# Kernel tuning notes

Measured on AMD Instinct MI355X. Metric: run time of the kernel, lower is better.

The kernel has to match this reference:

```python
import jax, jax.numpy as jnp
import numpy as np

N, B, NG = 12288, 8, 1536   # total nodes, graphs, nodes per graph
E, T, R, H = 49152, 9, 4, 128  # edges, node types, edge types, hidden

def setup_inputs() -> dict:
    key = jax.random.key(0)
    ks = jax.random.split(key, 24)
    s = 0.05
    inp = {
        'n_feats': jax.random.uniform(ks[0], (N, T), jnp.float32),
        'eps': jax.random.normal(ks[1], (N, H), jnp.float32),
        'edge_src': jax.random.randint(ks[2], (E,), 0, N, jnp.int32),
        'edge_dst': jax.random.randint(ks[3], (E,), 0, N, jnp.int32),
        'e_types': jax.random.randint(ks[4], (E,), 0, R, jnp.int32),
        # RelGraphConv params: per-relation weight, self-loop weight, bias
        'W1': jax.random.normal(ks[5], (R, T, H)) * s,  'Ws1': jax.random.normal(ks[6], (T, H)) * s,  'b1': jnp.zeros((H,)),
        'W2': jax.random.normal(ks[7], (R, H, H)) * s,  'Ws2': jax.random.normal(ks[8], (H, H)) * s,  'b2': jnp.zeros((H,)),
        'Wmu': jax.random.normal(ks[9], (R, H, H)) * s, 'Wsmu': jax.random.normal(ks[10], (H, H)) * s, 'bmu': jnp.zeros((H,)),
        'Wls': jax.random.normal(ks[11], (R, H, H)) * s, 'Wsls': jax.random.normal(ks[12], (H, H)) * s, 'bls': jnp.zeros((H,)),
        # decoder heads
        'Wnt': jax.random.normal(ks[13], (H, T)) * s, 'bnt': jnp.zeros((T,)),
        'we': jax.random.normal(ks[14], (3 * H + 2 * T,)) * s, 'be': jnp.zeros(()),
        'Wt': jax.random.normal(ks[15], (3 * H + 2 * T, R)) * s, 'bt': jnp.zeros((R,)),
    }
    return inp

def _relconv(h, W, Wself, b, edge_src, edge_dst, e_types):
    # per-relation transform then gather per edge: avoids [E,d,d] weight gather
    hr = jnp.einsum('nd,rdk->rnk', h, W)          # [R,N,H]
    msgs = hr[e_types, edge_src]                   # [E,H]
    agg = jax.ops.segment_sum(msgs, edge_dst, num_segments=N)
    return agg + h @ Wself + b

def reference(n_feats, eps, edge_src, edge_dst, e_types,
              W1, Ws1, b1, W2, Ws2, b2, Wmu, Wsmu, bmu, Wls, Wsls, bls,
              Wnt, bnt, we, be, Wt, bt):
    # ---- encode ----
    h = jax.nn.relu(_relconv(n_feats, W1, Ws1, b1, edge_src, edge_dst, e_types))
    h = jax.nn.relu(_relconv(h, W2, Ws2, b2, edge_src, edge_dst, e_types))
    mu = _relconv(h, Wmu, Wsmu, bmu, edge_src, edge_dst, e_types)
    logstd = _relconv(h, Wls, Wsls, bls, edge_src, edge_dst, e_types)
    z = mu + eps * jnp.exp(logstd)                 # reparameterize
    gz = z.reshape(B, NG, H).mean(axis=1)          # per-graph mean readout [B,H]

    # ---- decode (batched pairwise MLP) ----
    nt = z @ Wnt + bnt                             # [N,T]
    # edge_existence_fc on concat(u_z,u_t,v_z,v_t,gz) decomposes rank-1:
    wu_z, wu_t = we[:H], we[H:H + T]
    wv_z, wv_t = we[H + T:2 * H + T], we[2 * H + T:2 * H + 2 * T]
    wg = we[2 * H + 2 * T:]
    su = (z @ wu_z + nt @ wu_t).reshape(B, NG)     # [B,n]
    sv = (z @ wv_z + nt @ wv_t).reshape(B, NG)
    sg = gz @ wg + be                              # [B]
    exist = jax.nn.sigmoid(su[:, :, None] + sv[:, None, :] + sg[:, None, None])  # [B,n,n]

    Au = (z @ Wt[:H] + nt @ Wt[H:H + T]).reshape(B, NG, R)
    Av = (z @ Wt[H + T:2 * H + T] + nt @ Wt[2 * H + T:2 * H + 2 * T]).reshape(B, NG, R)
    Ag = gz @ Wt[2 * H + 2 * T:] + bt              # [B,R]
    type_logits = Au[:, :, None, :] + Av[:, None, :, :] + Ag[:, None, None, :]  # [B,n,n,R]

    pair_out = jnp.concatenate([exist[..., None], type_logits], axis=-1)  # [B,n,n,1+R]
    return pair_out, nt, mu, logstd
```

## Files before the change

kernel.cpp:

```cpp
#include <hip/hip_runtime.h>

#define NN 12288
#define TT 9
#define RR 4
#define HH 128
#define EE 49152
#define BB 8
#define NGG 1536
#define CAP 16

typedef unsigned short u16;
typedef float float4_t __attribute__((ext_vector_type(4)));
typedef __bf16 bf16x8 __attribute__((ext_vector_type(8)));
typedef unsigned short ushort8_t __attribute__((ext_vector_type(8)));

__device__ __forceinline__ u16 f2bf(float f) {
    union { float f; unsigned int u; } x; x.f = f;
    unsigned int r = x.u + 0x7FFFu + ((x.u >> 16) & 1u);
    return (u16)(r >> 16);
}
__device__ __forceinline__ float bf2f(u16 h) {
    union { unsigned int u; float f; } x; x.u = ((unsigned int)h) << 16; return x.f;
}

__global__ __launch_bounds__(256) void build_wts(
    const float* __restrict__ W1, const float* __restrict__ Ws1,
    const float* __restrict__ W2, const float* __restrict__ Ws2,
    const float* __restrict__ Wmu, const float* __restrict__ Wsmu,
    const float* __restrict__ Wls, const float* __restrict__ Wsls,
    u16* __restrict__ Bt1, u16* __restrict__ Bt2, u16* __restrict__ Bt34,
    int* __restrict__ cnt, float* __restrict__ gzacc)
{
    const int L1 = 128 * 64;
    const int L2 = L1 + 128 * 640;
    const int L3 = L2 + 256 * 640;
    const int L4 = L3 + NN * RR;
    const int L5 = L4 + BB * HH;
    int idx = blockIdx.x * 256 + threadIdx.x;
    if (idx < L1) {
        int k = idx >> 6, kk = idx & 63;
        float v = 0.f;
        if (kk < 36)      v = W1[kk * HH + k];
        else if (kk < 45) v = Ws1[(kk - 36) * HH + k];
        Bt1[k * 64 + kk] = f2bf(v);
    } else if (idx < L2) {
        int i2 = idx - L1;
        int k = i2 / 640, kk = i2 - k * 640;
        float v = (kk < 512) ? W2[kk * HH + k] : Ws2[(kk - 512) * HH + k];
        Bt2[k * 640 + kk] = f2bf(v);
    } else if (idx < L3) {
        int i3 = idx - L2;
        int j = i3 / 640, kk = i3 - j * 640;
        float v;
        if (j < 128) v = (kk < 512) ? Wmu[kk * HH + j] : Wsmu[(kk - 512) * HH + j];
        else { int jj = j - 128; v = (kk < 512) ? Wls[kk * HH + jj] : Wsls[(kk - 512) * HH + jj]; }
        Bt34[j * 640 + kk] = f2bf(v);
    } else if (idx < L4) {
        cnt[idx - L3] = 0;
    } else if (idx < L5) {
        gzacc[idx - L4] = 0.f;
    }
}

__global__ __launch_bounds__(256) void bucket_build(
    const int* __restrict__ esrc, const int* __restrict__ edst,
    const int* __restrict__ etyp, int* __restrict__ cnt, u16* __restrict__ buck)
{
    int e = blockIdx.x * 256 + threadIdx.x;
    if (e >= EE) return;
    int b = edst[e] * RR + etyp[e];
    int idx = atomicAdd(&cnt[b], 1);
    if (idx < CAP) buck[b * CAP + idx] = (u16)esrc[e];
}

__global__ __launch_bounds__(256) void gatherA1(
    const int* __restrict__ cnt, const u16* __restrict__ buck,
    const float* __restrict__ feats, u16* __restrict__ A)
{
    int idx = blockIdx.x * 256 + threadIdx.x;
    int n = idx >> 6, c = idx & 63;
    float v = 0.f;
    if (c < 36) {
        int r = c / 9, t = c - r * 9;
        int b = n * RR + r;
        int m = cnt[b]; m = m > CAP ? CAP : m;
        const u16* bp = buck + b * CAP;
        for (int i = 0; i < m; ++i) v += feats[(int)bp[i] * TT + t];
    } else if (c < 45) {
        v = feats[n * TT + (c - 36)];
    }
    A[(size_t)n * 64 + c] = f2bf(v);
}

__global__ __launch_bounds__(256) void gatherA2(
    const int* __restrict__ cnt, const u16* __restrict__ buck,
    const u16* __restrict__ h, u16* __restrict__ A)
{
    int n = blockIdx.x;
    u16* Ar = A + (size_t)n * 640;
    __shared__ int scnt[RR];
    __shared__ u16 ssrc[RR * CAP];
    if (threadIdx.x < RR) {
        int m = cnt[n * RR + threadIdx.x];
        scnt[threadIdx.x] = m > CAP ? CAP : m;
    }
    if (threadIdx.x < RR * CAP) ssrc[threadIdx.x] = buck[n * RR * CAP + threadIdx.x];
    __syncthreads();
    for (int c = threadIdx.x; c < 640; c += 256) {
        u16 v;
        if (c < 512) {
            int r = c >> 7, k = c & 127;
            float acc = 0.f;
            int m = scnt[r];
            for (int i = 0; i < m; ++i)
                acc += bf2f(h[(size_t)ssrc[r * CAP + i] * HH + k]);
            v = f2bf(acc);
        } else {
            v = h[(size_t)n * HH + (c - 512)];
        }
        Ar[c] = v;
    }
}

template <int MODE>
__global__ __launch_bounds__(256) void gemm_k(
    const u16* __restrict__ A, const u16* __restrict__ Bt, int K,
    const float* __restrict__ bias_a, const float* __restrict__ bias_b,
    u16* __restrict__ outb, float* __restrict__ outf_a, float* __restrict__ outf_b)
{
    __shared__ __align__(16) u16 lds_a[64 * 40];
    __shared__ __align__(16) u16 lds_b[128 * 40];
    const int tid = threadIdx.x;
    const int w = tid >> 6, lane = tid & 63;
    const int m0 = blockIdx.x * 64;
    const int n0 = blockIdx.y * 128;
    const int wm = (w & 1) * 32, wn = (w >> 1) * 64;
    const int lm = lane & 15, lq = lane >> 4;

    float4_t acc[2][4];
#pragma unroll
    for (int i = 0; i < 2; ++i)
#pragma unroll
        for (int j = 0; j < 4; ++j) acc[i][j] = (float4_t){0.f, 0.f, 0.f, 0.f};

    const int arow = tid >> 2, akc = (tid & 3) * 8;
    const int nsteps = K >> 5;
    for (int kt = 0; kt < nsteps; ++kt) {
        int k0 = kt * 32;
        *(ushort8_t*)&lds_a[arow * 40 + akc] =
            *(const ushort8_t*)&A[(size_t)(m0 + arow) * K + k0 + akc];
        {
            int c0 = tid;       int bn0 = c0 >> 2, bk0 = (c0 & 3) * 8;
            *(ushort8_t*)&lds_b[bn0 * 40 + bk0] =
                *(const ushort8_t*)&Bt[(size_t)(n0 + bn0) * K + k0 + bk0];
            int c1 = tid + 256; int bn1 = c1 >> 2, bk1 = (c1 & 3) * 8;
            *(ushort8_t*)&lds_b[bn1 * 40 + bk1] =
                *(const ushort8_t*)&Bt[(size_t)(n0 + bn1) * K + k0 + bk1];
        }
        __syncthreads();
        bf16x8 a0 = *(const bf16x8*)&lds_a[(wm + 0 * 16 + lm) * 40 + lq * 8];
        bf16x8 a1 = *(const bf16x8*)&lds_a[(wm + 1 * 16 + lm) * 40 + lq * 8];
        bf16x8 b0 = *(const bf16x8*)&lds_b[(wn + 0 * 16 + lm) * 40 + lq * 8];
        bf16x8 b1 = *(const bf16x8*)&lds_b[(wn + 1 * 16 + lm) * 40 + lq * 8];
        bf16x8 b2 = *(const bf16x8*)&lds_b[(wn + 2 * 16 + lm) * 40 + lq * 8];
        bf16x8 b3 = *(const bf16x8*)&lds_b[(wn + 3 * 16 + lm) * 40 + lq * 8];
        acc[0][0] = __builtin_amdgcn_mfma_f32_16x16x32_bf16(a0, b0, acc[0][0], 0, 0, 0);
        acc[0][1] = __builtin_amdgcn_mfma_f32_16x16x32_bf16(a0, b1, acc[0][1], 0, 0, 0);
        acc[0][2] = __builtin_amdgcn_mfma_f32_16x16x32_bf16(a0, b2, acc[0][2], 0, 0, 0);
        acc[0][3] = __builtin_amdgcn_mfma_f32_16x16x32_bf16(a0, b3, acc[0][3], 0, 0, 0);
        acc[1][0] = __builtin_amdgcn_mfma_f32_16x16x32_bf16(a1, b0, acc[1][0], 0, 0, 0);
        acc[1][1] = __builtin_amdgcn_mfma_f32_16x16x32_bf16(a1, b1, acc[1][1], 0, 0, 0);
        acc[1][2] = __builtin_amdgcn_mfma_f32_16x16x32_bf16(a1, b2, acc[1][2], 0, 0, 0);
        acc[1][3] = __builtin_amdgcn_mfma_f32_16x16x32_bf16(a1, b3, acc[1][3], 0, 0, 0);
        __syncthreads();
    }

#pragma unroll
    for (int i = 0; i < 2; ++i)
#pragma unroll
        for (int j = 0; j < 4; ++j) {
            int gn = n0 + wn + j * 16 + lm;
#pragma unroll
            for (int reg = 0; reg < 4; ++reg) {
                int gm = m0 + wm + i * 16 + lq * 4 + reg;
                float v = acc[i][j][reg];
                if (MODE == 0) {
                    v += bias_a[gn];
                    v = v > 0.f ? v : 0.f;
                    outb[(size_t)gm * HH + gn] = f2bf(v);
                } else {
                    if (gn < HH) {
                        outf_a[(size_t)gm * HH + gn] = v + bias_a[gn];
                    } else {
                        int g2 = gn - HH;
                        outf_b[(size_t)gm * HH + g2] = v + bias_b[g2];
                    }
                }
            }
        }
}

__global__ __launch_bounds__(256) void node_epi(
    const float* __restrict__ mu, const float* __restrict__ ls,
    const float* __restrict__ eps,
    const float* __restrict__ Wnt, const float* __restrict__ bnt,
    const float* __restrict__ we, const float* __restrict__ Wt,
    float* __restrict__ out_nt,
    float* __restrict__ su, float* __restrict__ sv,
    float* __restrict__ Au, float* __restrict__ Av,
    float* __restrict__ gzacc)
{
    __shared__ float zs[64][129];
    __shared__ float nts[64][10];
    __shared__ float red[256];
    const int nb = blockIdx.x * 64;
    const int tid = threadIdx.x;

    for (int i = tid; i < 64 * 32; i += 256) {
        int n = i >> 5, c4 = (i & 31) * 4;
        size_t g = (size_t)(nb + n) * HH + c4;
        float4_t m4 = *(const float4_t*)&mu[g];
        float4_t l4 = *(const float4_t*)&ls[g];
        float4_t e4 = *(const float4_t*)&eps[g];
        float* zp = &zs[n][c4];
#pragma unroll
        for (int j = 0; j < 4; ++j) zp[j] = m4[j] + e4[j] * __expf(l4[j]);
    }
    __syncthreads();

    for (int o = tid; o < 64 * TT; o += 256) {
        int n = o / TT, t = o - n * TT;
        float acc = bnt[t];
#pragma unroll 8
        for (int k = 0; k < HH; ++k) acc += zs[n][k] * Wnt[k * TT + t];
        nts[n][t] = acc;
        out_nt[(size_t)(nb + n) * TT + t] = acc;
    }
    __syncthreads();

    for (int o = tid; o < 64 * 10; o += 256) {
        int n = o / 10, j = o - n * 10;
        int zoff, toff;
        const float* wv;
        if (j == 0)      { zoff = 0;   toff = 128; wv = we; }
        else if (j == 1) { zoff = 137; toff = 265; wv = we; }
        else if (j < 6)  { zoff = 0;   toff = 128; wv = Wt + (j - 2); }
        else             { zoff = 137; toff = 265; wv = Wt + (j - 6); }
        int stride = (j < 2) ? 1 : 4;
        float acc = 0.f;
#pragma unroll 8
        for (int k = 0; k < HH; ++k) acc += zs[n][k] * wv[(zoff + k) * stride];
#pragma unroll
        for (int t = 0; t < TT; ++t) acc += nts[n][t] * wv[(toff + t) * stride];
        int gn = nb + n;
        if (j == 0)      su[gn] = acc;
        else if (j == 1) sv[gn] = acc;
        else if (j < 6)  Au[(size_t)gn * 4 + (j - 2)] = acc;
        else             Av[(size_t)gn * 4 + (j - 6)] = acc;
    }

    {
        int k = tid & 127, half = tid >> 7;
        float s = 0.f;
#pragma unroll 8
        for (int r = 0; r < 32; ++r) s += zs[half * 32 + r][k];
        red[tid] = s;
        __syncthreads();
        if (tid < 128) {
            int b = blockIdx.x / 24;
            atomicAdd(&gzacc[b * HH + tid], red[tid] + red[tid + 128]);
        }
    }
}

__global__ __launch_bounds__(128) void gz_final_kernel(
    const float* __restrict__ gzacc, const float* __restrict__ we,
    const float* __restrict__ Wt, const float* __restrict__ be,
    const float* __restrict__ bt, float* __restrict__ sg, float* __restrict__ Ag)
{
    int b = blockIdx.x, k = threadIdx.x;
    float gz = gzacc[b * HH + k] * (1.f / NGG);
    float vals[5] = { we[274 + k], Wt[(274 + k) * 4 + 0], Wt[(274 + k) * 4 + 1],
                      Wt[(274 + k) * 4 + 2], Wt[(274 + k) * 4 + 3] };
    __shared__ float red[128];
    for (int j = 0; j < 5; ++j) {
        red[k] = gz * vals[j];
        __syncthreads();
        for (int off = 64; off >= 1; off >>= 1) {
            if (k < off) red[k] += red[k + off];
            __syncthreads();
        }
        if (k == 0) {
            if (j == 0) sg[b] = red[0] + be[0];
            else        Ag[b * 4 + (j - 1)] = red[0] + bt[j - 1];
        }
        __syncthreads();
    }
}

__global__ __launch_bounds__(256) void pair_kernel(
    const float* __restrict__ su, const float* __restrict__ sv,
    const float* __restrict__ Au, const float* __restrict__ Av,
    const float* __restrict__ sg, const float* __restrict__ Ag,
    float* __restrict__ out)
{
    int row = blockIdx.x;
    int b = row / NGG;
    float su_u = su[row] + sg[b];
    float t0 = Au[(size_t)row * 4 + 0] + Ag[b * 4 + 0];
    float t1 = Au[(size_t)row * 4 + 1] + Ag[b * 4 + 1];
    float t2 = Au[(size_t)row * 4 + 2] + Ag[b * 4 + 2];
    float t3 = Au[(size_t)row * 4 + 3] + Ag[b * 4 + 3];
    const float* svb = sv + (size_t)b * NGG;
    const float* avb = Av + (size_t)b * NGG * 4;
    float4_t* od = (float4_t*)(out + (size_t)row * 7680);
    for (int d = threadIdx.x; d < 1920; d += 256) {
        float4_t vv;
#pragma unroll
        for (int j = 0; j < 4; ++j) {
            unsigned int e = (unsigned int)d * 4u + j;
            unsigned int v0 = (e * 52429u) >> 18;
            unsigned int c  = e - v0 * 5u;
            float f;
            if (c == 0u) { float x = su_u + svb[v0]; f = 1.f / (1.f + __expf(-x)); }
            else { float tv = (c == 1u) ? t0 : (c == 2u) ? t1 : (c == 3u) ? t2 : t3;
                   f = tv + avb[v0 * 4u + (c - 1u)]; }
            vv[j] = f;
        }
        __builtin_nontemporal_store(vv, &od[d]);
    }
}

extern "C" void kernel_launch(void* const* d_in, const int* in_sizes, int n_in,
                              void* d_out, int out_size, void* d_ws, size_t ws_size,
                              hipStream_t stream)
{
    const float* feats = (const float*)d_in[0];
    const float* eps   = (const float*)d_in[1];
    const int* esrc  = (const int*)d_in[2];
    const int* edst  = (const int*)d_in[3];
    const int* etyp  = (const int*)d_in[4];
    const float* W1    = (const float*)d_in[5];
    const float* Ws1   = (const float*)d_in[6];
    const float* b1    = (const float*)d_in[7];
    const float* W2    = (const float*)d_in[8];
    const float* Ws2   = (const float*)d_in[9];
    const float* b2    = (const float*)d_in[10];
    const float* Wmu   = (const float*)d_in[11];
    const float* Wsmu  = (const float*)d_in[12];
    const float* bmu   = (const float*)d_in[13];
    const float* Wls   = (const float*)d_in[14];
    const float* Wsls  = (const float*)d_in[15];
    const float* bls   = (const float*)d_in[16];
    const float* Wnt   = (const float*)d_in[17];
    const float* bnt   = (const float*)d_in[18];
    const float* we    = (const float*)d_in[19];
    const float* be    = (const float*)d_in[20];
    const float* Wt    = (const float*)d_in[21];
    const float* bt    = (const float*)d_in[22];

    char* p = (char*)d_ws;
    auto alloc = [&](size_t bytes) -> char* {
        char* r = p; p += (bytes + 255) & ~(size_t)255; return r;
    };
    u16*   Abuf  = (u16*)  alloc((size_t)NN * 640 * 2);
    u16*   hbf   = (u16*)  alloc((size_t)NN * HH * 2);
    int*   cnt   = (int*)  alloc((size_t)NN * RR * 4);
    u16*   buck  = (u16*)  alloc((size_t)NN * RR * CAP * 2);
    float* gzacc = (float*)alloc((size_t)BB * HH * 4);
    u16*   Bt1   = (u16*)  alloc(128 * 64 * 2);
    u16*   Bt2   = (u16*)  alloc(128 * 640 * 2);
    u16*   Bt34  = (u16*)  alloc(256 * 640 * 2);
    float* suA   = (float*)alloc(NN * 4);
    float* svA   = (float*)alloc(NN * 4);
    float* AuA   = (float*)alloc(NN * 4 * 4);
    float* AvA   = (float*)alloc(NN * 4 * 4);
    float* sgA   = (float*)alloc(BB * 4);
    float* AgA   = (float*)alloc(BB * 4 * 4);

    float* out = (float*)d_out;
    const size_t PO = (size_t)BB * NGG * NGG * 5;
    float* out_nt = out + PO;
    float* out_mu = out_nt + (size_t)NN * TT;
    float* out_ls = out_mu + (size_t)NN * HH;

    build_wts<<<1188, 256, 0, stream>>>(W1, Ws1, W2, Ws2, Wmu, Wsmu, Wls, Wsls,
                                        Bt1, Bt2, Bt34, cnt, gzacc);

    bucket_build<<<EE / 256, 256, 0, stream>>>(esrc, edst, etyp, cnt, buck);

    gatherA1<<<NN * 64 / 256, 256, 0, stream>>>(cnt, buck, feats, Abuf);
    gemm_k<0><<<dim3(NN / 64, 1), 256, 0, stream>>>(Abuf, Bt1, 64, b1, nullptr,
                                                    hbf, nullptr, nullptr);

    gatherA2<<<NN, 256, 0, stream>>>(cnt, buck, hbf, Abuf);
    gemm_k<0><<<dim3(NN / 64, 1), 256, 0, stream>>>(Abuf, Bt2, 640, b2, nullptr,
                                                    hbf, nullptr, nullptr);

    gatherA2<<<NN, 256, 0, stream>>>(cnt, buck, hbf, Abuf);
    gemm_k<1><<<dim3(NN / 64, 2), 256, 0, stream>>>(Abuf, Bt34, 640, bmu, bls,
                                                    nullptr, out_mu, out_ls);

    node_epi<<<NN / 64, 256, 0, stream>>>(out_mu, out_ls, eps, Wnt, bnt, we, Wt,
                                          out_nt, suA, svA, AuA, AvA, gzacc);

    gz_final_kernel<<<BB, 128, 0, stream>>>(gzacc, we, Wt, be, bt, sgA, AgA);
    pair_kernel<<<NN, 256, 0, stream>>>(suA, svA, AuA, AvA, sgA, AgA, out);
}
```

Baseline: 602.9 us.

## Fuse neighbor gather-aggregation into GEMM A-tile loads for all conv layers

Removes the separate gatherA1/gatherA2 kernels and the materialized [N,640] A buffer. Each GEMM block now stages bucket counts and source indices for its 64 rows in LDS and builds A tiles on the fly by summing neighbor rows of h, loading 8 bf16 values per neighbor. This avoids writing and re-reading the large A buffer and cuts kernel launches. In exchange the gather now sits inside the GEMM main loop without overlap and is redone by both column blocks of the mu/logstd GEMM. Ping-pong h buffers are added so a layer never reads the buffer it writes.

```diff
diff --git a/kernel.cpp b/kernel.cpp
--- a/kernel.cpp
+++ b/kernel.cpp
@@ -73,63 +73,114 @@
     if (idx < CAP) buck[b * CAP + idx] = (u16)esrc[e];
 }
 
-__global__ __launch_bounds__(256) void gatherA1(
+
+__global__ __launch_bounds__(256) void gemm_l1(
     const int* __restrict__ cnt, const u16* __restrict__ buck,
-    const float* __restrict__ feats, u16* __restrict__ A)
-{
-    int idx = blockIdx.x * 256 + threadIdx.x;
-    int n = idx >> 6, c = idx & 63;
-    float v = 0.f;
-    if (c < 36) {
-        int r = c / 9, t = c - r * 9;
-        int b = n * RR + r;
-        int m = cnt[b]; m = m > CAP ? CAP : m;
-        const u16* bp = buck + b * CAP;
-        for (int i = 0; i < m; ++i) v += feats[(int)bp[i] * TT + t];
-    } else if (c < 45) {
-        v = feats[n * TT + (c - 36)];
-    }
-    A[(size_t)n * 64 + c] = f2bf(v);
-}
-
-__global__ __launch_bounds__(256) void gatherA2(
+    const float* __restrict__ feats, const u16* __restrict__ Bt,
+    const float* __restrict__ bias, u16* __restrict__ outb)
+{
+    __shared__ __align__(16) u16 lds_a[64 * 40];
+    __shared__ __align__(16) u16 lds_b[128 * 40];
+    __shared__ int scnt[64 * RR];
+    __shared__ __align__(16) u16 ssrc[64 * RR * CAP];
+    const int tid = threadIdx.x;
+    const int w = tid >> 6, lane = tid & 63;
+    const int m0 = blockIdx.x * 64;
+    const int wm = (w & 1) * 32, wn = (w >> 1) * 64;
+    const int lm = lane & 15, lq = lane >> 4;
+
+    {
+        int m = cnt[m0 * RR + tid];
+        scnt[tid] = m > CAP ? CAP : m;
+        const ushort8_t* bs = (const ushort8_t*)(buck + (size_t)m0 * RR * CAP);
+        ushort8_t* bd = (ushort8_t*)ssrc;
+        bd[tid] = bs[tid];
+        bd[tid + 256] = bs[tid + 256];
+    }
+
+    float4_t acc[2][4];
+#pragma unroll
+    for (int i = 0; i < 2; ++i)
+#pragma unroll
+        for (int j = 0; j < 4; ++j) acc[i][j] = (float4_t){0.f, 0.f, 0.f, 0.f};
+
+    const int arow = tid >> 2, akc = (tid & 3) * 8;
+    __syncthreads();
+
+    for (int kt = 0; kt < 2; ++kt) {
+        int k0 = kt * 32;
+        {
+            ushort8_t av;
+#pragma unroll
+            for (int j = 0; j < 8; ++j) {
+                int c = k0 + akc + j;
+                float v = 0.f;
+                if (c < 36) {
+                    int r = (c >= 27) ? 3 : (c >= 18) ? 2 : (c >= 9) ? 1 : 0;
+                    int t = c - r * 9;
+                    int bi = arow * RR + r;
+                    int m = scnt[bi];
+                    const u16* sp = &ssrc[bi * CAP];
+                    for (int i = 0; i < m; ++i) v += feats[(int)sp[i] * TT + t];
+                } else if (c < 45) {
+                    v = feats[(m0 + arow) * TT + (c - 36)];
+                }
+                av[j] = f2bf(v);
+            }
+            *(ushort8_t*)&lds_a[arow * 40 + akc] = av;
+        }
+        {
+            int c0 = tid;       int bn0 = c0 >> 2, bk0 = (c0 & 3) * 8;
+            *(ushort8_t*)&lds_b[bn0 * 40 + bk0] =
+                *(const ushort8_t*)&Bt[(size_t)bn0 * 64 + k0 + bk0];
+            int c1 = tid + 256; int bn1 = c1 >> 2, bk1 = (c1 & 3) * 8;
+            *(ushort8_t*)&lds_b[bn1 * 40 + bk1] =
+                *(const ushort8_t*)&Bt[(size_t)bn1 * 64 + k0 + bk1];
+        }
+        __syncthreads();
+        bf16x8 a0 = *(const bf16x8*)&lds_a[(wm + 0 * 16 + lm) * 40 + lq * 8];
+        bf16x8 a1 = *(const bf16x8*)&lds_a[(wm + 1 * 16 + lm) * 40 + lq * 8];
+        bf16x8 b0 = *(const bf16x8*)&lds_b[(wn + 0 * 16 + lm) * 40 + lq * 8];
+        bf16x8 b1 = *(const bf16x8*)&lds_b[(wn + 1 * 16 + lm) * 40 + lq * 8];
+        bf16x8 b2 = *(const bf16x8*)&lds_b[(wn + 2 * 16 + lm) * 40 + lq * 8];
+        bf16x8 b3 = *(const bf16x8*)&lds_b[(wn + 3 * 16 + lm) * 40 + lq * 8];
+        acc[0][0] = __builtin_amdgcn_mfma_f32_16x16x32_bf16(a0, b0, acc[0][0], 0, 0, 0);
+        acc[0][1] = __builtin_amdgcn_mfma_f32_16x16x32_bf16(a0, b1, acc[0][1], 0, 0, 0);
+        acc[0][2] = __builtin_amdgcn_mfma_f32_16x16x32_bf16(a0, b2, acc[0][2], 0, 0, 0);
+        acc[0][3] = __builtin_amdgcn_mfma_f32_16x16x32_bf16(a0, b3, acc[0][3], 0, 0, 0);
+        acc[1][0] = __builtin_amdgcn_mfma_f32_16x16x32_bf16(a1, b0, acc[1][0], 0, 0, 0);
+        acc[1][1] = __builtin_amdgcn_mfma_f32_16x16x32_bf16(a1, b1, acc[1][1], 0, 0, 0);
+        acc[1][2] = __builtin_amdgcn_mfma_f32_16x16x32_bf16(a1, b2, acc[1][2], 0, 0, 0);
+        acc[1][3] = __builtin_amdgcn_mfma_f32_16x16x32_bf16(a1, b3, acc[1][3], 0, 0, 0);
+        __syncthreads();
+    }
+
+#pragma unroll
+    for (int i = 0; i < 2; ++i)
+#pragma unroll
+        for (int j = 0; j < 4; ++j) {
+            int gn = wn + j * 16 + lm;
+#pragma unroll
+            for (int reg = 0; reg < 4; ++reg) {
+                int gm = m0 + wm + i * 16 + lq * 4 + reg;
+                float v = acc[i][j][reg] + bias[gn];
+                v = v > 0.f ? v : 0.f;
+                outb[(size_t)gm * HH + gn] = f2bf(v);
+            }
+        }
+}
+
+template <int MODE>
+__global__ __launch_bounds__(256) void gemm_l23(
     const int* __restrict__ cnt, const u16* __restrict__ buck,
-    const u16* __restrict__ h, u16* __restrict__ A)
-{
-    int n = blockIdx.x;
-    u16* Ar = A + (size_t)n * 640;
-    __shared__ int scnt[RR];
-    __shared__ u16 ssrc[RR * CAP];
-    if (threadIdx.x < RR) {
-        int m = cnt[n * RR + threadIdx.x];
-        scnt[threadIdx.x] = m > CAP ? CAP : m;
-    }
-    if (threadIdx.x < RR * CAP) ssrc[threadIdx.x] = buck[n * RR * CAP + threadIdx.x];
-    __syncthreads();
-    for (int c = threadIdx.x; c < 640; c += 256) {
-        u16 v;
-        if (c < 512) {
-            int r = c >> 7, k = c & 127;
-            float acc = 0.f;
-            int m = scnt[r];
-            for (int i = 0; i < m; ++i)
-                acc += bf2f(h[(size_t)ssrc[r * CAP + i] * HH + k]);
-            v = f2bf(acc);
-        } else {
-            v = h[(size_t)n * HH + (c - 512)];
-        }
-        Ar[c] = v;
-    }
-}
-
-template <int MODE>
-__global__ __launch_bounds__(256) void gemm_k(
-    const u16* __restrict__ A, const u16* __restrict__ Bt, int K,
+    const u16* __restrict__ h, const u16* __restrict__ Bt,
     const float* __restrict__ bias_a, const float* __restrict__ bias_b,
     u16* __restrict__ outb, float* __restrict__ outf_a, float* __restrict__ outf_b)
 {
     __shared__ __align__(16) u16 lds_a[64 * 40];
     __shared__ __align__(16) u16 lds_b[128 * 40];
+    __shared__ int scnt[64 * RR];
+    __shared__ __align__(16) u16 ssrc[64 * RR * CAP];
     const int tid = threadIdx.x;
     const int w = tid >> 6, lane = tid & 63;
     const int m0 = blockIdx.x * 64;
@@ -137,6 +188,15 @@
     const int wm = (w & 1) * 32, wn = (w >> 1) * 64;
     const int lm = lane & 15, lq = lane >> 4;
 
+    {
+        int m = cnt[m0 * RR + tid];
+        scnt[tid] = m > CAP ? CAP : m;
+        const ushort8_t* bs = (const ushort8_t*)(buck + (size_t)m0 * RR * CAP);
+        ushort8_t* bd = (ushort8_t*)ssrc;
+        bd[tid] = bs[tid];
+        bd[tid + 256] = bs[tid + 256];
+    }
+
     float4_t acc[2][4];
 #pragma unroll
     for (int i = 0; i < 2; ++i)
@@ -144,11 +204,32 @@
         for (int j = 0; j < 4; ++j) acc[i][j] = (float4_t){0.f, 0.f, 0.f, 0.f};
 
     const int arow = tid >> 2, akc = (tid & 3) * 8;
-    const int nsteps = K >> 5;
-    for (int kt = 0; kt < nsteps; ++kt) {
+    const int K = 640;
+    __syncthreads();
+
+    for (int kt = 0; kt < 20; ++kt) {
         int k0 = kt * 32;
-        *(ushort8_t*)&lds_a[arow * 40 + akc] =
-            *(const ushort8_t*)&A[(size_t)(m0 + arow) * K + k0 + akc];
+        {
+            int k = k0 + akc;
+            ushort8_t av;
+            if (k < 512) {
+                int r = k >> 7, kk = k & 127;
+                int bi = arow * RR + r;
+                int m = scnt[bi];
+                const u16* sp = &ssrc[bi * CAP];
+                float a[8] = {0.f, 0.f, 0.f, 0.f, 0.f, 0.f, 0.f, 0.f};
+                for (int i = 0; i < m; ++i) {
+                    ushort8_t hv = *(const ushort8_t*)&h[(size_t)sp[i] * HH + kk];
+#pragma unroll
+                    for (int j = 0; j < 8; ++j) a[j] += bf2f(hv[j]);
+                }
+#pragma unroll
+                for (int j = 0; j < 8; ++j) av[j] = f2bf(a[j]);
+            } else {
+                av = *(const ushort8_t*)&h[(size_t)(m0 + arow) * HH + (k - 512)];
+            }
+            *(ushort8_t*)&lds_a[arow * 40 + akc] = av;
+        }
         {
             int c0 = tid;       int bn0 = c0 >> 2, bk0 = (c0 & 3) * 8;
             *(ushort8_t*)&lds_b[bn0 * 40 + bk0] =
@@ -363,8 +444,8 @@
     auto alloc = [&](size_t bytes) -> char* {
         char* r = p; p += (bytes + 255) & ~(size_t)255; return r;
     };
-    u16*   Abuf  = (u16*)  alloc((size_t)NN * 640 * 2);
-    u16*   hbf   = (u16*)  alloc((size_t)NN * HH * 2);
+    u16*   hbf1  = (u16*)  alloc((size_t)NN * HH * 2);
+    u16*   hbf2  = (u16*)  alloc((size_t)NN * HH * 2);
     int*   cnt   = (int*)  alloc((size_t)NN * RR * 4);
     u16*   buck  = (u16*)  alloc((size_t)NN * RR * CAP * 2);
     float* gzacc = (float*)alloc((size_t)BB * HH * 4);
@@ -389,17 +470,13 @@
 
     bucket_build<<<EE / 256, 256, 0, stream>>>(esrc, edst, etyp, cnt, buck);
 
-    gatherA1<<<NN * 64 / 256, 256, 0, stream>>>(cnt, buck, feats, Abuf);
-    gemm_k<0><<<dim3(NN / 64, 1), 256, 0, stream>>>(Abuf, Bt1, 64, b1, nullptr,
-                                                    hbf, nullptr, nullptr);
-
-    gatherA2<<<NN, 256, 0, stream>>>(cnt, buck, hbf, Abuf);
-    gemm_k<0><<<dim3(NN / 64, 1), 256, 0, stream>>>(Abuf, Bt2, 640, b2, nullptr,
-                                                    hbf, nullptr, nullptr);
-
-    gatherA2<<<NN, 256, 0, stream>>>(cnt, buck, hbf, Abuf);
-    gemm_k<1><<<dim3(NN / 64, 2), 256, 0, stream>>>(Abuf, Bt34, 640, bmu, bls,
-                                                    nullptr, out_mu, out_ls);
+    gemm_l1<<<NN / 64, 256, 0, stream>>>(cnt, buck, feats, Bt1, b1, hbf1);
+
+    gemm_l23<0><<<dim3(NN / 64, 1), 256, 0, stream>>>(cnt, buck, hbf1, Bt2, b2, nullptr,
+                                                      hbf2, nullptr, nullptr);
+
+    gemm_l23<1><<<dim3(NN / 64, 2), 256, 0, stream>>>(cnt, buck, hbf2, Bt34, bmu, bls,
+                                                      nullptr, out_mu, out_ls);
 
     node_epi<<<NN / 64, 256, 0, stream>>>(out_mu, out_ls, eps, Wnt, bnt, we, Wt,
                                           out_nt, suA, svA, AuA, AvA, gzacc);
```

Measured after the change: 600.2 us. About the same (-0.5%).
